# Kernel optimization log

Hardware: AMD Instinct MI355X
Metric: run time of the kernel (lower is better)

The kernel has to match this reference:

```python
import jax, jax.numpy as jnp
import numpy as np

B, C, H, W = 8, 64, 112, 112
F, KH, KW = 128, 3, 3
SPARSITY = 0.7  # fraction of kernel entries zeroed (Uniform connector)


def setup_inputs() -> dict:
    key = jax.random.key(0)
    k1, k2, k3 = jax.random.split(key, 3)
    inputs = jax.random.normal(k1, (B, C, H, W), dtype=jnp.float32)
    fan_in = C * KH * KW
    limit = float(np.sqrt(6.0 / (F + fan_in)))
    vals = jax.random.uniform(k2, (F, fan_in), minval=-limit, maxval=limit, dtype=jnp.float32)
    mask = (jax.random.uniform(k3, (F, fan_in)) >= SPARSITY).astype(jnp.float32)
    kernel = vals * mask  # dense representation of the sparse kernel
    return {"inputs": inputs, "kernel": kernel}


def _extract_patches(x, kh, kw):
    # x: [B, S1, S2, C]; VALID padding, stride 1, rate 1.
    # Matches tf.image.extract_patches depth ordering: (pi, pj) major, channel minor.
    Bb, S1, S2, Cc = x.shape
    o1, o2 = S1 - kh + 1, S2 - kw + 1
    pats = jnp.stack(
        [x[:, i:i + o1, j:j + o2, :] for i in range(kh) for j in range(kw)],
        axis=3,
    )  # [B, o1, o2, kh*kw, C]
    return pats.reshape(Bb, o1, o2, kh * kw * Cc)


def reference(inputs, kernel):
    # inputs: [B, C, H, W] (NCHW, per bias_add data_format and build())
    x = jnp.transpose(inputs, (0, 3, 2, 1))  # [B, W, H, C] (perm [0,3,2,1] in original)
    p = _extract_patches(x, KH, KW)          # [B, oW, oH, KH*KW*C]
    # spmm(kernel [F, K], im2col [K, B*oW*oH]) expressed as a single contraction
    out = jnp.einsum('bwhk,fk->bfwh', p, kernel)  # [B, F, oW, oH]
    return out
```

## Files before the change

### kernel.cpp

```cpp
#include <hip/hip_runtime.h>

typedef unsigned short u16;
typedef unsigned int u32;
typedef _Float16 f16x8 __attribute__((ext_vector_type(8)));
typedef float f32x4 __attribute__((ext_vector_type(4)));

#define B_ 8
#define C_ 64
#define H_ 112
#define W_ 112
#define HW_ 12544
#define F_ 128
#define OH_ 110
#define OW_ 110
#define OWOH 12100
#define NPOS 96800
#define KK_ 576
#define NT_ 384
#define NWGF 506
#define OCTSTRIDE 802816
#define AELEMS 73728
#define AHALF 36864

__device__ __forceinline__ void gl_lds16(const void* g, void* l) {
  __builtin_amdgcn_global_load_lds((const __attribute__((address_space(1))) void*)g,
                                   (__attribute__((address_space(3))) void*)l,
                                   16, 0, 0);
}

__global__ __launch_bounds__(256) void prep_all(const float* __restrict__ in,
                                                const float* __restrict__ k,
                                                u16* __restrict__ xT,
                                                u16* __restrict__ kT) {
  const int bid = blockIdx.x;
  const int tid = threadIdx.x;
  if (bid >= 896) {
    const int base = (bid - 896) * 2048;
#pragma unroll
    for (int t = 0; t < 8; ++t) {
      int idx = base + t * 256 + tid;
      int ko = idx >> 10;
      int rem = idx & 1023;
      int f = rem >> 3;
      int c = rem & 7;
      _Float16 h = (_Float16)k[f * KK_ + ko * 8 + c];
      kT[idx] = __builtin_bit_cast(u16, h);
    }
    return;
  }
  __shared__ float tile[8][8][113];
  const int b = bid / 112;
  const int r = bid % 112;
  const int oct = r / 14;
  const int hs = (r % 14) * 8;

  for (int idx = tid; idx < 8 * 8 * 112; idx += 256) {
    int c = idx / 896;
    int rem = idx - c * 896;
    int h = rem / 112;
    int w = rem - h * 112;
    tile[c][h][w] = in[(((size_t)(b * 64 + oct * 8 + c)) * 112 + (hs + h)) * 112 + w];
  }
  __syncthreads();

  for (int idx = tid; idx < 896; idx += 256) {
    int w = idx >> 3;
    int h = idx & 7;
    f16x8 v;
#pragma unroll
    for (int c = 0; c < 8; ++c) v[c] = (_Float16)tile[c][h][w];
    size_t o = ((((size_t)oct * B_ + b) * W_ + w) * H_ + (hs + h)) * 8;
    *(f16x8*)(xT + o) = v;
  }
}

__global__ __launch_bounds__(256, 2) void conv_mfma(
    const u16* __restrict__ xT, const u16* __restrict__ kT,
    float* __restrict__ out) {
  __shared__ u16 lds[AHALF];

  const int tid = threadIdx.x;
  const int wave = tid >> 6;
  const int lane = tid & 63;

  const int orig = blockIdx.x;
  const int xcd = orig & 7;
  const int sub = orig >> 3;
  const int wg = (xcd < 2 ? xcd * 64 : 128 + (xcd - 2) * 63) + sub;
  const int nblk = wg >> 1;
  const int fh = wg & 1;
  const int n0 = nblk * NT_ + wave * 96;

  const int l15 = lane & 15;
  const int l4 = lane >> 4;

  int posOff[6];
#pragma unroll
  for (int ni = 0; ni < 6; ++ni) {
    int n = n0 + ni * 16 + l15;
    if (n >= NPOS) n = 0;
    int b = n / OWOH;
    int r = n - b * OWOH;
    int w = r / OH_;
    int h = r - w * OH_;
    posOff[ni] = ((b * W_ + w) * H_ + h) * 8;
  }
  const int l4Off = l4 * OCTSTRIDE;

  f16x8 b0[6];
#pragma unroll
  for (int ni = 0; ni < 6; ++ni) b0[ni] = *(const f16x8*)(xT + posOff[ni] + l4Off);

#pragma unroll
  for (int it = 0; it < 18; ++it) {
    const int m = it * 256 + tid;
    const int src = ((m >> 6) << 10) + (fh << 9) + ((m & 63) << 3);
    gl_lds16(kT + src, (char*)lds + m * 16);
  }
  __syncthreads();

  f32x4 acc[4][6] = {};

#pragma unroll
  for (int s = 0; s < 18; ++s) {
    const int tap = s >> 1;
    const int half = s & 1;
    const int i = tap / 3;
    const int j = tap - i * 3;
    const int sShift = (i * H_ + j) * 8 + half * 4 * OCTSTRIDE;

    f16x8 bh[6];
    if (s == 0) {
#pragma unroll
      for (int ni = 0; ni < 6; ++ni) bh[ni] = b0[ni];
    } else {
#pragma unroll
      for (int ni = 0; ni < 6; ++ni)
        bh[ni] = *(const f16x8*)(xT + posOff[ni] + l4Off + sShift);
    }

    f16x8 ah[4];
    const int ko = s * 4 + l4;
    const int aBase = ((ko << 6) + l15) * 8;
#pragma unroll
    for (int mi = 0; mi < 4; ++mi) ah[mi] = *(const f16x8*)&lds[aBase + mi * 128];

#pragma unroll
    for (int mi = 0; mi < 4; ++mi)
#pragma unroll
      for (int ni = 0; ni < 6; ++ni)
        acc[mi][ni] = __builtin_amdgcn_mfma_f32_16x16x32_f16(ah[mi], bh[ni], acc[mi][ni], 0, 0, 0);
  }

#pragma unroll
  for (int ni = 0; ni < 6; ++ni) {
    int n = n0 + ni * 16 + l15;
    if (n >= NPOS) continue;
    int b = n / OWOH;
    int r = n - b * OWOH;
    int w = r / OH_;
    int h = r - w * OH_;
    float* op = out + ((size_t)(b * F_) * OW_ + w) * OH_ + h;
#pragma unroll
    for (int mi = 0; mi < 4; ++mi) {
      int fbase = fh * 64 + mi * 16 + l4 * 4;
#pragma unroll
      for (int qq = 0; qq < 4; ++qq) {
        op[(size_t)(fbase + qq) * OWOH] = acc[mi][ni][qq];
      }
    }
  }
}

__global__ void naive_conv(const float* __restrict__ in, const float* __restrict__ ker,
                           float* __restrict__ out) {
  int idx = blockIdx.x * 256 + threadIdx.x;
  const int total = B_ * F_ * OW_ * OH_;
  if (idx >= total) return;
  int h = idx % OH_;
  int w = (idx / OH_) % OW_;
  int f = (idx / (OW_ * OH_)) % F_;
  int b = idx / (F_ * OW_ * OH_);
  float s = 0.f;
  for (int tap = 0; tap < 9; ++tap) {
    int i = tap / 3, j = tap % 3;
    const float* ip = in + ((size_t)b * C_ * H_ + (h + j)) * W_ + (w + i);
    const float* kp = ker + (size_t)f * KK_ + tap * C_;
    for (int c = 0; c < C_; ++c) s += ip[(size_t)c * HW_] * kp[c];
  }
  out[idx] = s;
}

extern "C" void kernel_launch(void* const* d_in, const int* in_sizes, int n_in,
                              void* d_out, int out_size, void* d_ws, size_t ws_size,
                              hipStream_t stream) {
  const float* in = (const float*)d_in[0];
  const float* ker = (const float*)d_in[1];
  float* out = (float*)d_out;

  const size_t xElems = (size_t)B_ * H_ * W_ * C_;
  const size_t need = (xElems + AELEMS) * 2;

  if (ws_size < need) {
    int total = B_ * F_ * OW_ * OH_;
    naive_conv<<<(total + 255) / 256, 256, 0, stream>>>(in, ker, out);
    return;
  }

  u16* xT = (u16*)d_ws;
  u16* kT = xT + xElems;

  prep_all<<<932, 256, 0, stream>>>(in, ker, xT, kT);
  conv_mfma<<<NWGF, 256, 0, stream>>>(xT, kT, out);
}
```

Measured before the change: 37.26 us.

## Switch conv MFMA from 16x16x32 to 32x32x16 tiles with relaid-out operands

Replaces the 4x6 grid of 16x16x32 f16 MFMAs per wave with a 2x3 grid of 32x32x16 MFMAs, issued twice per step to cover the same K. The kernel-weight prep layout, LDS A-fragment indexing, global B-fragment loads and output scatter are all reorganized to match the 32-lane operand mapping. The aim is fewer MFMA issues and fewer fragment loads for the same tile, trading for a different accumulator register layout and store pattern.

```diff
diff --git a/kernel.cpp b/kernel.cpp
--- a/kernel.cpp
+++ b/kernel.cpp
@@ -3,7 +3,7 @@
 typedef unsigned short u16;
 typedef unsigned int u32;
 typedef _Float16 f16x8 __attribute__((ext_vector_type(8)));
-typedef float f32x4 __attribute__((ext_vector_type(4)));
+typedef float f32x16 __attribute__((ext_vector_type(16)));
 
 #define B_ 8
 #define C_ 64
@@ -39,11 +39,11 @@
 #pragma unroll
     for (int t = 0; t < 8; ++t) {
       int idx = base + t * 256 + tid;
-      int ko = idx >> 10;
-      int rem = idx & 1023;
-      int f = rem >> 3;
-      int c = rem & 7;
-      _Float16 h = (_Float16)k[f * KK_ + ko * 8 + c];
+      int c = idx & 7;
+      int f = (idx >> 3) & 127;
+      int hf = (idx >> 10) & 1;
+      int ko16 = idx >> 11;
+      _Float16 h = (_Float16)k[f * KK_ + ko16 * 16 + hf * 8 + c];
       kT[idx] = __builtin_bit_cast(u16, h);
     }
     return;
@@ -82,6 +82,8 @@
   const int tid = threadIdx.x;
   const int wave = tid >> 6;
   const int lane = tid & 63;
+  const int l31 = lane & 31;
+  const int hi = lane >> 5;
 
   const int orig = blockIdx.x;
   const int xcd = orig & 7;
@@ -91,13 +93,10 @@
   const int fh = wg & 1;
   const int n0 = nblk * NT_ + wave * 96;
 
-  const int l15 = lane & 15;
-  const int l4 = lane >> 4;
-
-  int posOff[6];
-#pragma unroll
-  for (int ni = 0; ni < 6; ++ni) {
-    int n = n0 + ni * 16 + l15;
+  int posOff[3];
+#pragma unroll
+  for (int ni = 0; ni < 3; ++ni) {
+    int n = n0 + ni * 32 + l31;
     if (n >= NPOS) n = 0;
     int b = n / OWOH;
     int r = n - b * OWOH;
@@ -105,21 +104,23 @@
     int h = r - w * OH_;
     posOff[ni] = ((b * W_ + w) * H_ + h) * 8;
   }
-  const int l4Off = l4 * OCTSTRIDE;
 
   f16x8 b0[6];
 #pragma unroll
-  for (int ni = 0; ni < 6; ++ni) b0[ni] = *(const f16x8*)(xT + posOff[ni] + l4Off);
+  for (int ni = 0; ni < 3; ++ni)
+#pragma unroll
+    for (int t = 0; t < 2; ++t)
+      b0[ni * 2 + t] = *(const f16x8*)(xT + (t * 2 + hi) * OCTSTRIDE + posOff[ni]);
 
 #pragma unroll
   for (int it = 0; it < 18; ++it) {
     const int m = it * 256 + tid;
-    const int src = ((m >> 6) << 10) + (fh << 9) + ((m & 63) << 3);
-    gl_lds16(kT + src, (char*)lds + m * 16);
+    const int src = ((m >> 6) << 7) + (fh << 6) + (m & 63);
+    gl_lds16(kT + src * 8, (char*)lds + m * 16);
   }
   __syncthreads();
 
-  f32x4 acc[4][6] = {};
+  f32x16 acc[2][3] = {};
 
 #pragma unroll
   for (int s = 0; s < 18; ++s) {
@@ -127,34 +128,41 @@
     const int half = s & 1;
     const int i = tap / 3;
     const int j = tap - i * 3;
-    const int sShift = (i * H_ + j) * 8 + half * 4 * OCTSTRIDE;
+    const int sShift = (i * H_ + j) * 8;
 
     f16x8 bh[6];
     if (s == 0) {
 #pragma unroll
-      for (int ni = 0; ni < 6; ++ni) bh[ni] = b0[ni];
+      for (int q = 0; q < 6; ++q) bh[q] = b0[q];
     } else {
 #pragma unroll
-      for (int ni = 0; ni < 6; ++ni)
-        bh[ni] = *(const f16x8*)(xT + posOff[ni] + l4Off + sShift);
+      for (int ni = 0; ni < 3; ++ni)
+#pragma unroll
+        for (int t = 0; t < 2; ++t)
+          bh[ni * 2 + t] = *(const f16x8*)(xT + (half * 4 + t * 2 + hi) * OCTSTRIDE +
+                                           posOff[ni] + sShift);
     }
 
     f16x8 ah[4];
-    const int ko = s * 4 + l4;
-    const int aBase = ((ko << 6) + l15) * 8;
-#pragma unroll
-    for (int mi = 0; mi < 4; ++mi) ah[mi] = *(const f16x8*)&lds[aBase + mi * 128];
-
-#pragma unroll
-    for (int mi = 0; mi < 4; ++mi)
-#pragma unroll
-      for (int ni = 0; ni < 6; ++ni)
-        acc[mi][ni] = __builtin_amdgcn_mfma_f32_16x16x32_f16(ah[mi], bh[ni], acc[mi][ni], 0, 0, 0);
-  }
-
-#pragma unroll
-  for (int ni = 0; ni < 6; ++ni) {
-    int n = n0 + ni * 16 + l15;
+#pragma unroll
+    for (int t = 0; t < 2; ++t)
+#pragma unroll
+      for (int mi = 0; mi < 2; ++mi)
+        ah[t * 2 + mi] = *(const f16x8*)&lds[((((s * 2 + t) * 2 + hi) << 6) + mi * 32 + l31) * 8];
+
+#pragma unroll
+    for (int t = 0; t < 2; ++t)
+#pragma unroll
+      for (int mi = 0; mi < 2; ++mi)
+#pragma unroll
+        for (int ni = 0; ni < 3; ++ni)
+          acc[mi][ni] = __builtin_amdgcn_mfma_f32_32x32x16_f16(ah[t * 2 + mi], bh[ni * 2 + t],
+                                                               acc[mi][ni], 0, 0, 0);
+  }
+
+#pragma unroll
+  for (int ni = 0; ni < 3; ++ni) {
+    int n = n0 + ni * 32 + l31;
     if (n >= NPOS) continue;
     int b = n / OWOH;
     int r = n - b * OWOH;
@@ -162,11 +170,12 @@
     int h = r - w * OH_;
     float* op = out + ((size_t)(b * F_) * OW_ + w) * OH_ + h;
 #pragma unroll
-    for (int mi = 0; mi < 4; ++mi) {
-      int fbase = fh * 64 + mi * 16 + l4 * 4;
-#pragma unroll
-      for (int qq = 0; qq < 4; ++qq) {
-        op[(size_t)(fbase + qq) * OWOH] = acc[mi][ni][qq];
+    for (int mi = 0; mi < 2; ++mi) {
+      const int fbase = fh * 64 + mi * 32 + 4 * hi;
+#pragma unroll
+      for (int reg = 0; reg < 16; ++reg) {
+        int f = fbase + (reg & 3) + 8 * (reg >> 2);
+        op[(size_t)f * OWOH] = acc[mi][ni][reg];
       }
     }
   }
```

Result: slower. 38.80 us (+4.1%).
